# Optimization experiments

Measured on AMD Instinct MI355X. Metric: run time of the kernel, lower is better.

The kernel has to match this reference:

```python
import jax, jax.numpy as jnp
import numpy as np

B, S, D = 8, 1024, 768
H, DQK, DV = 12, 64, 64
DHEAD = 2 * DQK + DV  # 192, interleaved per-head qkv layout
DOUT = 768


def setup_inputs() -> dict:
    key = jax.random.key(0)
    k1, k2, k3, k4 = jax.random.split(key, 4)
    x = jax.random.normal(k1, (B, S, D), dtype=jnp.float32)
    w_qkv = jax.random.normal(k2, (D, H * DHEAD), dtype=jnp.float32) * (D ** -0.5)
    w_out = jax.random.normal(k3, (H * DV, DOUT), dtype=jnp.float32) * ((H * DV) ** -0.5)
    b_out = jax.random.normal(k4, (DOUT,), dtype=jnp.float32) * 0.02
    return {"x": x, "w_qkv": w_qkv, "w_out": w_out, "b_out": b_out}


def reference(x, w_qkv, w_out, b_out):
    scale = DQK ** -0.5
    # Interleaved per-head layout: [B,S,H,DHEAD] then split into q|k|v blocks.
    qkv = (x @ w_qkv).reshape(B, S, H, DHEAD)
    q = qkv[..., :DQK]                 # [B,S,H,DQK]
    k = qkv[..., DQK:2 * DQK]          # [B,S,H,DQK]
    v = qkv[..., 2 * DQK:]             # [B,S,H,DV]
    scores = jnp.einsum("bshd,bthd->bhst", q, k) * scale  # [B,H,S,S]
    attn = jax.nn.softmax(scores, axis=-1)
    out = jnp.einsum("bhst,bthd->bshd", attn, v)           # [B,S,H,DV]
    out = out.reshape(B, S, H * DV)
    return out @ w_out + b_out
```

## Files before the change

kernel.cpp:

```cpp
#include <hip/hip_runtime.h>
#include <hip/hip_bf16.h>
#include <cstdint>

namespace {

constexpr int kB = 8;
constexpr int kS = 1024;
constexpr int kD = 768;
constexpr int kH = 12;
constexpr int kDH = 192;
constexpr int kNQ = kH * kDH;
constexpr int kNK = kH * 128;
constexpr int kM = kB * kS;
constexpr int kDO = 768;

using f32x4 = __attribute__((ext_vector_type(4))) float;
using f32x16 = __attribute__((ext_vector_type(16))) float;
using s16x8 = __attribute__((ext_vector_type(8))) short;
using u16x8 = __attribute__((ext_vector_type(8))) unsigned short;
using u16x4 = __attribute__((ext_vector_type(4))) unsigned short;

__device__ __forceinline__ unsigned short f2bf(float f) {
  union { float f; uint32_t u; } v; v.f = f;
  uint32_t u = v.u;
  u += 0x7FFFu + ((u >> 16) & 1u);
  return (unsigned short)(u >> 16);
}

__device__ __forceinline__ unsigned packbf(float a, float b) {
  return (unsigned)f2bf(a) | ((unsigned)f2bf(b) << 16);
}

__device__ __forceinline__ void load_lds16(const void* g, void* l) {
  __builtin_amdgcn_global_load_lds((__attribute__((address_space(1))) void*)g,
                                   (__attribute__((address_space(3))) void*)l,
                                   16, 0, 0);
}

__device__ __forceinline__ s16x8 repack8(int hi, float p0, float p1, float p2, float p3,
                                         float p4, float p5, float p6, float p7) {
  unsigned x0 = packbf(p0, p1);
  unsigned x1 = packbf(p2, p3);
  unsigned x2 = packbf(p4, p5);
  unsigned x3 = packbf(p6, p7);
  unsigned y0 = (unsigned)__shfl_xor((int)x0, 32, 64);
  unsigned y1 = (unsigned)__shfl_xor((int)x1, 32, 64);
  unsigned y2 = (unsigned)__shfl_xor((int)x2, 32, 64);
  unsigned y3 = (unsigned)__shfl_xor((int)x3, 32, 64);
  union { unsigned u[4]; s16x8 v; } r;
  r.u[0] = hi ? y2 : x0;
  r.u[1] = hi ? y3 : x1;
  r.u[2] = hi ? x2 : y0;
  r.u[3] = hi ? x3 : y1;
  return r.v;
}


__global__ __launch_bounds__(256) void cvt_x_kernel(const float* __restrict__ in,
                                                    unsigned short* __restrict__ out) {
  int i = (blockIdx.x * 256 + threadIdx.x) * 8;
  float4 a = *(const float4*)(in + i);
  float4 b = *(const float4*)(in + i + 4);
  u16x8 o;
  o[0] = f2bf(a.x); o[1] = f2bf(a.y); o[2] = f2bf(a.z); o[3] = f2bf(a.w);
  o[4] = f2bf(b.x); o[5] = f2bf(b.y); o[6] = f2bf(b.z); o[7] = f2bf(b.w);
  *(u16x8*)(out + i) = o;
}

__global__ __launch_bounds__(256) void cvt_transpose_kernel(const float* __restrict__ w,
                                                            unsigned short* __restrict__ wt,
                                                            int K, int N) {
  __shared__ float tile[32][33];
  int k0 = blockIdx.x * 32, n0 = blockIdx.y * 32;
  int tx = threadIdx.x & 31, ty = threadIdx.x >> 5;
  #pragma unroll
  for (int r = 0; r < 32; r += 8)
    tile[ty + r][tx] = w[(size_t)(k0 + ty + r) * N + n0 + tx];
  __syncthreads();
  #pragma unroll
  for (int r = 0; r < 32; r += 8)
    wt[(size_t)(n0 + ty + r) * K + k0 + tx] = f2bf(tile[tx][ty + r]);
}

template <int MODE>
__global__ __launch_bounds__(256, 2) void gemm_bt_kernel(
    const unsigned short* __restrict__ A,
    const unsigned short* __restrict__ Bt,
    void* __restrict__ Cout,
    unsigned short* __restrict__ Vtg,
    const float* __restrict__ bias,
    int M, int N, int K) {
  __shared__ alignas(16) unsigned short Al[128 * 64];
  __shared__ alignas(16) unsigned short Bl[128 * 64];
  const int nT = N >> 7;
  const int tm = blockIdx.x / nT, tn = blockIdx.x % nT;
  const int tid = threadIdx.x;
  const int w = tid >> 6, l = tid & 63;
  const int wr = w >> 1, wc = w & 1;
  const int la = l & 15, g = l >> 4;
  const int sr = l >> 3, sc = l & 7;

  f32x4 acc[4][4] = {};
  const unsigned short* Ag = A + (size_t)(tm * 128) * K;
  const unsigned short* Bg = Bt + (size_t)(tn * 128) * K;

  for (int k0 = 0; k0 < K; k0 += 64) {
    #pragma unroll
    for (int j = 0; j < 4; ++j) {
      int row = w * 32 + j * 8 + sr;
      load_lds16(Ag + (size_t)row * K + k0 + sc * 8, &Al[row * 64 + sc * 8]);
      load_lds16(Bg + (size_t)row * K + k0 + sc * 8, &Bl[row * 64 + sc * 8]);
    }
    __syncthreads();
    #pragma unroll
    for (int kk = 0; kk < 2; ++kk) {
      s16x8 af[4], bfv[4];
      #pragma unroll
      for (int i = 0; i < 4; ++i)
        af[i] = *(const s16x8*)&Al[(wr * 64 + i * 16 + la) * 64 + kk * 32 + g * 8];
      #pragma unroll
      for (int j = 0; j < 4; ++j)
        bfv[j] = *(const s16x8*)&Bl[(wc * 64 + j * 16 + la) * 64 + kk * 32 + g * 8];
      #pragma unroll
      for (int i = 0; i < 4; ++i)
        #pragma unroll
        for (int j = 0; j < 4; ++j)
          acc[i][j] = __builtin_amdgcn_mfma_f32_16x16x32_bf16(af[i], bfv[j], acc[i][j], 0, 0, 0);
    }
    __syncthreads();
  }

  #pragma unroll
  for (int i = 0; i < 4; ++i) {
    int row0 = tm * 128 + wr * 64 + i * 16 + g * 4;
    #pragma unroll
    for (int j = 0; j < 4; ++j) {
      int col = tn * 128 + wc * 64 + j * 16 + la;
      if (MODE == 0) {
        int h = col / kDH, colm = col % kDH;
        if (colm < 128) {
          unsigned short* C = (unsigned short*)Cout;
          float sc2 = (colm < 64) ? 0.125f : 1.0f;
          int ncol = h * 128 + colm;
          #pragma unroll
          for (int r = 0; r < 4; ++r)
            C[(size_t)(row0 + r) * kNK + ncol] = f2bf(acc[i][j][r]

 * sc2);
        } else {
          int d = colm - 128;
          int bb = row0 >> 10, t = row0 & 1023;
          u16x4 pv;
          #pragma unroll
          for (int r = 0; r < 4; ++r) pv[r] = f2bf(acc[i][j][r]);
          *(u16x4*)&Vtg[((size_t)(bb * kH + h) * 64 + d) * kS + t] = pv;
        }
      } else {
        float* C = (float*)Cout;
        float bv = bias[col];
        #pragma unroll
        for (int r = 0; r < 4; ++r)
          C[(size_t)(row0 + r) * N + col] = acc[i][j][r] + bv;
      }
    }
  }
}

__global__ __launch_bounds__(256, 3) void attn_kernel(
    const unsigned short* __restrict__ qk,
    const unsigned short* __restrict__ Vtg,
    unsigned short* __restrict__ Ab) {
  const int id = blockIdx.x;
  const int b = id & 7;
  const int h = (id >> 3) % kH;
  const int qb = id / (kH * 8);
  const int tid = threadIdx.x;
  const int w = tid >> 6, l = tid & 63;
  const int q0 = l & 31, hi = l >> 5;

  __shared__ alignas(16) unsigned short Kl[64 * 64];
  __shared__ alignas(16) unsigned short Vl[64 * 64];

  const size_t base_bs = (size_t)b * kS;
  const size_t qrow0 = base_bs + (size_t)qb * 128;
  const size_t myq = qrow0 + w * 32 + q0;

  s16x8 qf[4];
  {
    const unsigned short* qp = qk + myq * kNK + h * 128 + hi * 8;
    #pragma unroll
    for (int kg = 0; kg < 4; ++kg) qf[kg] = *(const s16x8*)(qp + kg * 16);
  }

  const int c0 = w * 64 + l;
  const int c1 = 256 + w * 64 + l;
  const int r0 = c0 >> 3, cc0 = (c0 & 7) ^ (r0 & 7);
  const int r1 = c1 >> 3, cc1 = (c1 & 7) ^ (r1 & 7);
  const unsigned short* Kg = qk + base_bs * kNK + h * 128 + 64;
  const unsigned short* Vg = Vtg + (size_t)(b * kH + h) * 64 * kS;

  const float LOG2E = 1.44269504088896340736f;
  float m2 = -1e30f;
  float lrow = 0.f;
  f32x16 oacc[2] = {};

  for (int kt = 0; kt < 16; ++kt) {
    __syncthreads();
    load_lds16(Kg + (size_t)(kt * 64 + r0) * kNK + cc0 * 8, &Kl[c0 * 8]);
    load_lds16(Kg + (size_t)(kt * 64 + r1) * kNK + cc1 * 8, &Kl[c1 * 8]);
    load_lds16(Vg + (size_t)r0 * kS + kt * 64 + cc0 * 8, &Vl[c0 * 8]);
    load_lds16(Vg + (size_t)r1 * kS + kt * 64 + cc1 * 8, &Vl[c1 * 8]);
    __syncthreads();

    f32x16 sacc[2] = {};
    #pragma unroll
    for (int tb = 0; tb < 2; ++tb) {
      const int tl = tb * 32 + q0, xr = tl & 7;
      #pragma unroll
      for (int kg = 0; kg < 4; ++kg) {
        s16x8 kf = *(const s16x8*)&Kl[tl * 64 + (((kg * 2 + hi) ^ xr) * 8)];
        sacc[tb] = __builtin_amdgcn_mfma_f32_32x32x16_bf16(kf, qf[kg], sacc[tb], 0, 0, 0);
      }
    }

    float mx[16];
    #pragma unroll
    for (int r = 0; r < 16; ++r) mx[r] = fmaxf(sacc[0][r], sacc[1][r]);
    #pragma unroll
    for (int s2 = 8; s2 >= 1; s2 >>= 1)
      #pragma unroll
      for (int r = 0; r < s2; ++r) mx[r] = fmaxf(mx[r], mx[r + s2]);
    float pmax = fmaxf(mx[0], __shfl_xor(mx[0], 32, 64));
    float rx2 = pmax * LOG2E;
    if (!__all(rx2 - m2 <= 11.5416f)) {
      float m2n = fmaxf(m2, rx2);
      float corr = exp2f(m2 - m2n);
      m2 = m2n;
      lrow *= corr;
      #pragma unroll
      for (int db = 0; db < 2; ++db)
        #pragma unroll
        for (int r = 0; r < 16; ++r) oacc[db][r] *= corr;
    }

    float p[32];
    #pragma unroll
    for (int tb = 0; tb < 2; ++tb)
      #pragma unroll
      for (int r = 0; r < 16; ++r)
        p[tb * 16 + r] = exp2f(fmaf(sacc[tb][r], LOG2E, -m2));

    float sm[16];
    #pragma unroll
    for (int r = 0; r < 16; ++r) sm[r] = p[r] + p[16 + r];
    #pragma unroll
    for (int s2 = 8; s2 >= 1; s2 >>= 1)
      #pragma unroll
      for (int r = 0; r < s2; ++r) sm[r] += sm[r + s2];
    lrow += sm[0] + __shfl_xor(sm[0], 32, 64);

    s16x8 pb0 = repack8(hi, p[0], p[1], p[2], p[3], p[4], p[5], p[6], p[7]);
    s16x8 pb1 = repack8(hi, p[8], p[9], p[10], p[11], p[12], p[13], p[14], p[15]);
    s16x8 pb2 = repack8(hi, p[16], p[17], p[18], p[19], p[20], p[21], p[22], p[23]);
    s16x8 pb3 = repack8(hi, p[24], p[25], p[26], p[27], p[28], p[29], p[30], p[31]);

    #pragma unroll
    for (int db = 0; db < 2; ++db) {
      const int dl = db * 32 + q0, xr = dl & 7;
      s16x8 v0 = *(const s16x8*)&Vl[dl * 64 + (((0 + hi) ^ xr) * 8)];
      s16x8 v1 = *(const s16x8*)&Vl[dl * 64 + (((2 + hi) ^ xr) * 8)];
      s16x8 v2 = *(const s16x8*)&Vl[dl * 64 + (((4 + hi) ^ xr) * 8)];
      s16x8 v3 = *(const s16x8*)&Vl[dl * 64 + (((6 + hi) ^ xr) * 8)];
      oacc[db] = __builtin_amdgcn_mfma_f32_32x32x16_bf16(v0, pb0, oacc[db], 0, 0, 0);
      oacc[db] = __builtin_amdgcn_mfma_f32_32x32x16_bf16(v1, pb1, oacc[db], 0, 0, 0);
      oacc[db] = __builtin_amdgcn_mfma_f32_32x32x16_bf16(v2, pb2, oacc[db], 0, 0, 0);
      oacc[db] = __builtin_amdgcn_mfma_f32_32x32x16_bf16(v3, pb3, oacc[db], 0, 0, 0);
    }
  }

  float inv = 1.0f / lrow;
  unsigned short* dst = Ab + myq * (size_t)(kH * 64) + h * 64;
  #pragma unroll
  for (int db = 0; db < 2; ++db)
    #pragma unroll
    for (int rq = 0; rq < 4; ++rq) {
      u16x4 pv;
      #pragma unroll
      for (int j = 0; j < 4; ++j) pv[j] = f2bf(oacc[db][rq * 4 + j] * inv);
      *(u16x4*)&dst[db * 32 + rq * 8 + hi * 4] = pv;
    }
}

}

extern "C" void kernel_launch(void* const* d_in, const int* in_sizes, int n_in,
                              void* d_out, int out_size, void* d_ws, size_t ws_size,
                              hipStream_t stream) {
  (void)in_sizes; (void)n_in; (void)out_size; (void)ws_size;
  const float* x = (const float*)d_in[0];
  const float* w_qkv = (const float*)d_in[1];
  const float* w_out = (const float*)d_in[2];
  const float* b_out = (const float*)d_in[3];

  unsigned short* Xb = (unsigned short*)d_ws;
  unsigned short* WqT = Xb + (size_t)kM * kD;
  unsigned short* WoT = WqT + (size_t)kNQ * kD;
  unsigned short* QK = WoT + (size_t)kDO * kDO;
  unsigned short* Vtg = QK + (size_t)kM * kNK;
  unsigned short* Ab = Vtg + (size_t)kB * kH * 64 * kS;

  cvt_x_kernel<<<dim3((kM * kD) / (256 * 8)), dim3(256), 0, stream>>>(x, Xb);
  cvt_transpose_kernel<<<dim3(kD / 32, kNQ / 32), dim3(256), 0, stream>>>(w_qkv, WqT, kD, kNQ);
  cvt_transpose_kernel<<<dim3(kDO / 32, kDO / 32), dim3(256), 0, stream>>>(w_out, WoT, kDO, kDO);

  gemm_bt_kernel<0><<<dim3((kM / 128) * (kNQ / 128)), dim3(256), 0, stream>>>(
      Xb, WqT, (void*)QK, Vtg, nullptr, kM, kNQ, kD);

  attn_kernel<<<dim3((kS / 128) * kH * kB), dim3(256), 0, stream>>>(QK, Vtg, Ab);

  gemm_bt_kernel<1><<<dim3((kM / 128) * (kDO / 128)), dim3(256), 0, stream>>>(
      Ab, WoT, d_out, nullptr, b_out, kM, kDO, kH * 64);
}
```

Baseline: 211.0 us.

## Double-buffer K/V tiles in attention kernel to overlap loads with compute

Result: no change. 212.8 us (+0.9%).

```diff
diff --git a/kernel.cpp b/kernel.cpp
--- a/kernel.cpp
+++ b/kernel.cpp
@@ -144,9 +144,7 @@
           int ncol = h * 128 + colm;
           #pragma unroll
           for (int r = 0; r < 4; ++r)
-            C[(size_t)(row0 + r) * kNK + ncol] = f2bf(acc[i][j][r]
-
- * sc2);
+            C[(size_t)(row0 + r) * kNK + ncol] = f2bf(acc[i][j][r] * sc2);
         } else {
           int d = colm - 128;
           int bb = row0 >> 10, t = row0 & 1023;
@@ -178,8 +176,8 @@
   const int w = tid >> 6, l = tid & 63;
   const int q0 = l & 31, hi = l >> 5;
 
-  __shared__ alignas(16) unsigned short Kl[64 * 64];
-  __shared__ alignas(16) unsigned short Vl[64 * 64];
+  __shared__ alignas(16) unsigned short Kl[2][64 * 64];
+  __shared__ alignas(16) unsigned short Vl[2][64 * 64];
 
   const size_t base_bs = (size_t)b * kS;
   const size_t qrow0 = base_bs + (size_t)qb * 128;
@@ -199,18 +197,29 @@
   const unsigned short* Kg = qk + base_bs * kNK + h * 128 + 64;
   const unsigned short* Vg = Vtg + (size_t)(b * kH + h) * 64 * kS;
 
+  auto STAGE = [&](int buf, int kt) {
+    load_lds16(Kg + (size_t)(kt * 64 + r0) * kNK + cc0 * 8, &Kl[buf][c0 * 8]);
+    load_lds16(Kg + (size_t)(kt * 64 + r1) * kNK + cc1 * 8, &Kl[buf][c1 * 8]);
+    load_lds16(Vg + (size_t)r0 * kS + kt * 64 + cc0 * 8, &Vl[buf][c0 * 8]);
+    load_lds16(Vg + (size_t)r1 * kS + kt * 64 + cc1 * 8, &Vl[buf][c1 * 8]);
+  };
+
   const float LOG2E = 1.44269504088896340736f;
   float m2 = -1e30f;
   float lrow = 0.f;
   f32x16 oacc[2] = {};
 
+  STAGE(0, 0);
+  asm volatile("s_waitcnt vmcnt(0)" ::: "memory");
+  __builtin_amdgcn_s_barrier();
+  __builtin_amdgcn_sched_barrier(0);
+
+  int cur = 0;
   for (int kt = 0; kt < 16; ++kt) {
-    __syncthreads();
-    load_lds16(Kg + (size_t)(kt * 64 + r0) * kNK + cc0 * 8, &Kl[c0 * 8]);
-    load_lds16(Kg + (size_t)(kt * 64 + r1) * kNK + cc1 * 8, &Kl[c1 * 8]);
-    load_lds16(Vg + (size_t)r0 * kS + kt * 64 + cc0 * 8, &Vl[c0 * 8]);
-    load_lds16(Vg + (size_t)r1 * kS + kt * 64 + cc1 * 8, &Vl[c1 * 8]);
-    __syncthreads();
+    if (kt < 15) STAGE(cur ^ 1, kt + 1);
+
+    const unsigned short* Kc = &Kl[cur][0];
+    const unsigned short* Vc = &Vl[cur][0];
 
     f32x16 sacc[2] = {};
     #pragma unroll
@@ -218,7 +227,7 @@
       const int tl = tb * 32 + q0, xr = tl & 7;
       #pragma unroll
       for (int kg = 0; kg < 4; ++kg) {
-        s16x8 kf = *(const s16x8*)&Kl[tl * 64 + (((kg * 2 + hi) ^ xr) * 8)];
+        s16x8 kf = *(const s16x8*)&Kc[tl * 64 + (((kg * 2 + hi) ^ xr) * 8)];
         sacc[tb] = __builtin_amdgcn_mfma_f32_32x32x16_bf16(kf, qf[kg], sacc[tb], 0, 0, 0);
       }
     }
@@ -267,15 +276,21 @@
     #pragma unroll
     for (int db = 0; db < 2; ++db) {
       const int dl = db * 32 + q0, xr = dl & 7;
-      s16x8 v0 = *(const s16x8*)&Vl[dl * 64 + (((0 + hi) ^ xr) * 8)];
-      s16x8 v1 = *(const s16x8*)&Vl[dl * 64 + (((2 + hi) ^ xr) * 8)];
-      s16x8 v2 = *(const s16x8*)&Vl[dl * 64 + (((4 + hi) ^ xr) * 8)];
-      s16x8 v3 = *(const s16x8*)&Vl[dl * 64 + (((6 + hi) ^ xr) * 8)];
+      s16x8 v0 = *(const s16x8*)&Vc[dl * 64 + (((0 + hi) ^ xr) * 8)];
+      s16x8 v1 = *(const s16x8*)&Vc[dl * 64 + (((2 + hi) ^ xr) * 8)];
+      s16x8 v2 = *(const s16x8*)&Vc[dl * 64 + (((4 + hi) ^ xr) * 8)];
+      s16x8 v3 = *(const s16x8*)&Vc[dl * 64 + (((6 + hi) ^ xr) * 8)];
       oacc[db] = __builtin_amdgcn_mfma_f32_32x32x16_bf16(v0, pb0, oacc[db], 0, 0, 0);
       oacc[db] = __builtin_amdgcn_mfma_f32_32x32x16_bf16(v1, pb1, oacc[db], 0, 0, 0);
       oacc[db] = __builtin_amdgcn_mfma_f32_32x32x16_bf16(v2, pb2, oacc[db], 0, 0, 0);
       oacc[db] = __builtin_amdgcn_mfma_f32_32x32x16_bf16(v3, pb3, oacc[db], 0, 0, 0);
     }
+
+    __builtin_amdgcn_sched_barrier(0);
+    asm volatile("s_waitcnt vmcnt(0)" ::: "memory");
+    __builtin_amdgcn_s_barrier();
+    __builtin_amdgcn_sched_barrier(0);
+    cur ^= 1;
   }
 
   float inv = 1.0f / lrow;
```
